# Performance work log

Measured on AMD Instinct MI355X. Metric: run time of the kernel, lower is better.

The kernel has to match this reference:

```python
import jax, jax.numpy as jnp
import numpy as np

B, N, DEG = 16, 2048, 16          # graphs, nodes per graph, avg out-degree
C_IN, HID, K = 64, 128, 32        # in_channels, hidden_channels, out_channels (clusters)
NT = B * N                        # total nodes
E = NT * DEG                      # total edges
GN_EPS = 1e-5


def setup_inputs() -> dict:
    key = jax.random.key(0)
    ks = jax.random.split(key, 6)
    x = jax.random.normal(ks[0], (NT, C_IN), jnp.float32)
    # within-graph random edges (sorted batch => node i belongs to graph i // N)
    src_l = jax.random.randint(ks[1], (E,), 0, N)
    dst_l = jax.random.randint(ks[2], (E,), 0, N)
    gid = jnp.repeat(jnp.arange(B, dtype=jnp.int32), N * DEG)
    edge_index = jnp.stack([gid * N + src_l, gid * N + dst_l]).astype(jnp.int32)
    batch = jnp.repeat(jnp.arange(B, dtype=jnp.int32), N)
    return dict(
        x=x, edge_index=edge_index, batch=batch,
        gn_weight=jnp.ones((C_IN,), jnp.float32),
        gn_bias=jnp.zeros((C_IN,), jnp.float32),
        gn_mean_scale=jnp.ones((C_IN,), jnp.float32),
        w1=jax.random.normal(ks[3], (C_IN, HID), jnp.float32) / np.float32(np.sqrt(C_IN)),
        b1=jnp.zeros((HID,), jnp.float32),
        w2=jax.random.normal(ks[4], (HID, K), jnp.float32) / np.float32(np.sqrt(HID)),
        b2=jnp.zeros((K,), jnp.float32),
    )


def reference(x, gn_weight, gn_bias, gn_mean_scale, w1, b1, w2, b2, edge_index, batch):
    # ---- GraphNorm (per-graph mean/var with learnable mean scale) ----
    ones_n = jnp.ones((NT,), x.dtype)
    cnt = jax.ops.segment_sum(ones_n, batch, num_segments=B)[:, None]        # [B,1]
    mean = jax.ops.segment_sum(x, batch, num_segments=B) / cnt              # [B,C]
    xm = x - gn_mean_scale * mean[batch]
    var = jax.ops.segment_sum(xm * xm, batch, num_segments=B) / cnt         # [B,C]
    h = gn_weight * xm / jnp.sqrt(var + GN_EPS)[batch] + gn_bias            # [NT,C_IN]

    # ---- GCNConv (add self-loops, symmetric D^-1/2 (A+I) D^-1/2) ----
    src, dst = edge_index[0], edge_index[1]
    loop = jnp.arange(NT, dtype=src.dtype)
    src_l = jnp.concatenate([src, loop])
    dst_l = jnp.concatenate([dst, loop])
    deg = jax.ops.segment_sum(jnp.ones_like(src_l, x.dtype), dst_l, num_segments=NT)
    dinv = jnp.where(deg > 0, jax.lax.rsqrt(deg), 0.0)
    norm = dinv[src_l] * dinv[dst_l]                                        # [E+NT]
    hw = h @ w1                                                             # [NT,HID]
    h = jax.ops.segment_sum(norm[:, None] * hw[src_l], dst_l, num_segments=NT) + b1
    h = jax.nn.selu(h)

    # ---- to_dense_batch / to_dense_adj (uniform graph sizes -> mask all True) ----
    xd = h.reshape(B, N, HID)                                               # [B,N,F]
    adj = jnp.zeros((B, N, N), x.dtype).at[batch[src], src % N, dst % N].add(1.0)

    # ---- DMoNPooling ----
    s = jax.nn.softmax(xd @ w2 + b2, axis=-1)                               # [B,N,K]
    out = jax.nn.selu(jnp.einsum('bnk,bnf->bkf', s, xd))                    # [B,K,F]
    sta = jnp.einsum('bnk,bnm->bkm', s, adj)                                # [B,K,N]
    out_adj = jnp.einsum('bkm,bml->bkl', sta, s)                            # [B,K,K]

    degrees = adj.sum(-1)                                                   # [B,N]
    m = degrees.sum(-1) / 2                                                 # [B]
    ca = jnp.einsum('bnk,bn->bk', s, degrees)                               # [B,K]
    normalizer = ca[:, :, None] * ca[:, None, :] / 2 / m[:, None, None]
    spectral_loss = (-jnp.einsum('bkk->b', out_adj - normalizer) / (2 * m)).mean()

    ss = jnp.einsum('bnk,bnl->bkl', s, s)                                   # [B,K,K]
    ss_fro = jnp.sqrt(jnp.sum(ss * ss, axis=(-2, -1), keepdims=True))
    eye = jnp.eye(K, dtype=x.dtype)
    diff = ss / ss_fro - eye / jnp.sqrt(jnp.float32(K))
    ortho_loss = jnp.sqrt(jnp.sum(diff * diff, axis=(-2, -1))).mean()

    cluster_size = s.sum(1)                                                 # [B,K]
    cluster_loss = (jnp.linalg.norm(cluster_size, axis=1) / N
                    * jnp.sqrt(jnp.float32(K)) - 1).mean()
    # (coarsened-adj renormalization in DMoNPooling is unused by Net's outputs)

    return jax.nn.log_softmax(out, axis=-1), spectral_loss + ortho_loss + cluster_loss, s
```

## Files before the change

kernel.cpp:

```cpp
#include <hip/hip_runtime.h>
#include <cmath>

static constexpr int B_  = 16;
static constexpr int N_  = 2048;
static constexpr int NT_ = 32768;
static constexpr int E_  = 524288;

static constexpr size_t OFF_HSC    = 0;
static constexpr size_t OFF_XD     = 2097152;
static constexpr size_t OFF_SWS    = 6291456;
static constexpr size_t OFF_PART   = 7340032;
static constexpr size_t OFF_GSP    = 9437184;
static constexpr size_t OFF_GSP2   = 9445376;
static constexpr size_t OFF_SSP    = 9453568;
static constexpr size_t OFF_CAP    = 9977856;
static constexpr size_t OFF_CSP    = 9994240;
static constexpr size_t OFF_SPECP  = 10010624;
static constexpr size_t OFF_DINV   = 10011136;
static constexpr size_t OFF_IHIN   = 10043904;
static constexpr size_t OFF_IHOUT  = 10306048;
static constexpr size_t OFF_ICURS  = 10568192;
static constexpr size_t OFF_IROWS  = 10830336;
static constexpr size_t OFF_ICNTO  = 10863108;
static constexpr size_t OFF_IESRC  = 10895876;

__device__ __forceinline__ float selu_f(float x) {
  return 1.0507009873554805f * (x > 0.f ? x : 1.6732632423543772f * expm1f(x));
}

__device__ __forceinline__ float block_sum_bcast(float v, float* sm) {
  int lane = threadIdx.x & 63, w = threadIdx.x >> 6;
#pragma unroll
  for (int off = 32; off; off >>= 1) v += __shfl_down(v, off);
  __syncthreads();
  if (lane == 0) sm[w] = v;
  __syncthreads();
  return sm[0] + sm[1] + sm[2] + sm[3];
}

__global__ __launch_bounds__(1024) void k_count(const int* ei, const float* x,
                                                int* histin, int* histout,
                                                float* gsp, float* gsp2) {
  __shared__ int hin[2048], hout[2048];
  __shared__ float l1[16][64], l2[16][64];
  int blk = blockIdx.x;
  int tid = threadIdx.x;
  if (blk < 128) {
    int g = blk >> 3, p = blk & 7;
    int nbase = g * 2048, ebase = g * 32768 + p * 4096;
    hin[tid] = 0; hin[tid + 1024] = 0;
    hout[tid] = 0; hout[tid + 1024] = 0;
    __syncthreads();
#pragma unroll
    for (int it = 0; it < 4; it++) {
      int e = ebase + it * 1024 + tid;
      int s = ei[e], d = ei[E_ + e];
      atomicAdd(&hout[s - nbase], 1);
      atomicAdd(&hin[d - nbase], 1);
    }
    __syncthreads();
    histin[blk * 2048 + tid] = hin[tid];
    histin[blk * 2048 + tid + 1024] = hin[tid + 1024];
    histout[blk * 2048 + tid] = hout[tid];
    histout[blk * 2048 + tid + 1024] = hout[tid + 1024];
  } else {
    int gi = blk - 128;
    int b = gi >> 3, chunk = gi & 7;
    int c = tid & 63, r = tid >> 6;
    float s = 0.f, s2 = 0.f;
    const float* xb = x + ((size_t)b * N_ + (size_t)chunk * 256) * 64;
    for (int n = r; n < 256; n += 16) {
      float v = xb[n * 64 + c];
      s += v; s2 += v * v;
    }
    l1[r][c] = s; l2[r][c] = s2;
    __syncthreads();
    if (r == 0) {
      float t1 = 0.f, t2 = 0.f;
#pragma unroll
      for (int i = 0; i < 16; i++) { t1 += l1[i][c]; t2 += l2[i][c]; }
      gsp[gi * 64 + c] = t1;
      gsp2[gi * 64 + c] = t2;
    }
  }
}

__global__ __launch_bounds__(1024) void k_scan(const int* histin, const int* histout,
                                               int* rows, int* cursp, int* cout_,
                                               float* dinv) {
  __shared__ int sb[1024];
  int g = blockIdx.x, tid = threadIdx.x;
  int nbase = g * 2048, ebase = g * 32768;
  int n0 = 2 * tid, n1 = 2 * tid + 1;
  int h0[8], h1[8];
  int a = 0, b = 0, o0 = 0, o1 = 0;
#pragma unroll
  for (int p = 0; p < 8; p++) {
    h0[p] = histin[(g * 8 + p) * 2048 + n0];
    h1[p] = histin[(g * 8 + p) * 2048 + n1];
    a += h0[p]; b += h1[p];
    o0 += histout[(g * 8 + p) * 2048 + n0];
    o1 += histout[(g * 8 + p) * 2048 + n1];
  }
  sb[tid] = a + b;
  __syncthreads();
  for (int off = 1; off < 1024; off <<= 1) {
    int add = (tid >= off) ? sb[tid - off] : 0;
    __syncthreads();
    sb[tid] += add;
    __syncthreads();
  }
  int pref = (tid > 0) ? sb[tid - 1] : 0;
  int r0 = ebase + pref, r1 = r0 + a;
  rows[nbase + n0] = r0;
  rows[nbase + n1] = r1;
  dinv[nbase + n0] = rsqrtf((float)(a + 1));
  dinv[nbase + n1] = rsqrtf((float)(b + 1));
  cout_[nbase + n0] = o0;
  cout_[nbase + n1] = o1;
  int run0 = r0, run1 = r1;
#pragma unroll
  for (int p = 0; p < 8; p++) {
    cursp[(g * 8 + p) * 2048 + n0] = run0; run0 += h0[p];
    cursp[(g * 8 + p) * 2048 + n1] = run1; run1 += h1[p];
  }
  if (g == 15 && tid == 1023) rows[NT_] = E_;
}

__global__ __launch_bounds__(256) void k_prepb(const float* x, const float* gsp,
                                               const float* gsp2, const float* gw,
                                               const float* gb, const float* gms,
                                               const float* dinv, float* hsc,
                                               const int* ei, const int* cursp,
                                               int* esrc) {
  __shared__ float shs[64], scs[64];
  __shared__ int cur[2048];
  int tid = threadIdx.x;
  int blk = blockIdx.x;
  if (blk < 2048) {
    int bgr = blk >> 7;
    if (tid < 64) {
      float s = 0.f, s2 = 0.f;
#pragma unroll
      for (int c8 = 0; c8 < 8; c8++) {
        s  += gsp[(bgr * 8 + c8) * 64 + tid];
        s2 += gsp2[(bgr * 8 + c8) * 64 + tid];
      }
      float mean = s * (1.f / 2048.f);
      float a = gms[tid];
      float var = s2 * (1.f / 2048.f) - (2.f * a - a * a) * mean * mean;
      shs[tid] = a * mean;
      scs[tid] = gw[tid] * rsqrtf(var + 1e-5f);
    }
    __syncthreads();
    int idx = blk * 256 + tid;
    int node = idx >> 4, g4 = (idx & 15) * 4;
    float di = dinv[node];
    float4 xv = *(const float4*)&x[(size_t)node * 64 + g4];
    float4 bb = *(const float4*)&gb[g4];
    float4 o;
    o.x = ((xv.x - shs[g4])     * scs[g4]     + bb.x) * di;
    o.y = ((xv.y - shs[g4 + 1]) * scs[g4 + 1] + bb.y) * di;
    o.z = ((xv.z - shs[g4 + 2]) * scs[g4 + 2] + bb.z) * di;
    o.w = ((xv.w - shs[g4 + 3]) * scs[g4 + 3] + bb.w) * di;
    *(float4*)&hsc[(size_t)node * 64 + g4] = o;
  } else {
    int bb = blk - 2048;
    int g = bb >> 3, p = bb & 7;
    int nbase = g * 2048;
    int ebase = g * 32768 + p * 4096;
    for (int i = tid; i < 2048; i += 256) cur[i] = cursp[bb * 2048 + i];
    __syncthreads();
#pragma unroll
    for (int it = 0; it < 16; it++) {
      int e = ebase + it * 256 + tid;
      int s = ei[e], d = ei[E_ + e];
      int pos = atomicAdd(&cur[d - nbase], 1);
      esrc[pos] = s;
    }
  }
}

__global__ __launch_bounds__(256) void k_mm1(const float* hsc, const float* dinv,
                                             const int* rows, const int* esrc,
                                             const float* w1, const float* b1,
                                             float* xd) {
  __shared__ float at[32 * 65];
  int tid = threadIdx.x;
  int n0 = blockIdx.x * 32;
  int wv = tid >> 6, c = tid & 63;
#pragma unroll 1
  for (int i = 0; i < 8; i++) {
    int nn = i * 4 + wv;
    int node = n0 + nn;
    int e0 = rows[node], e1 = rows[node + 1];
    float dd = dinv[node];
    float acc = hsc[(size_t)node * 64 + c];
    for (int e = e0; e < e1; e += 8) {
      int sidx[8]; float wt[8], hv[8];
#pragma unroll
      for (int j = 0; j < 8; j++) {
        int ee = e + j;
        sidx[j] = esrc[ee < e1 ? ee : e0];
        wt[j] = (ee < e1) ? 1.f : 0.f;
      }
#pragma unroll
      for (int j = 0; j < 8; j++) hv[j] = hsc[(size_t)sidx[j] * 64 + c];
#pragma unroll
      for (int j = 0; j < 8; j++) acc += wt[j] * hv[j];
    }
    at[nn * 65 + c] = dd * acc;
  }
  __syncthreads();
  int tx = tid & 31, ty = tid >> 5;
  int f0 = tx * 4, nn = ty * 4;
  float acc[4][4] = {};
  for (int k = 0; k < 64; k++) {
    float4 wvv = *(const float4*)&w1[k * 128 + f0];
#pragma unroll
    for (int i = 0; i < 4; i++) {
      float av = at[(nn + i) * 65 + k];
      acc[i][0] += av * wvv.x; acc[i][1] += av * wvv.y;
      acc[i][2] += av * wvv.z; acc[i][3] += av * wvv.w;
    }
  }
  float4 bv = *(const float4*)&b1[f0];
#pragma unroll
  for (int i = 0; i < 4; i++) {
    float4 o;
    o.x = selu_f(acc[i][0] + bv.x);
    o.y = selu_f(acc[i][1] + bv.y);
    o.z = selu_f(acc[i][2] + bv.z);
    o.w = selu_f(acc[i][3] + bv.w);
    *(float4*)&xd[(size_t)(n0 + nn + i) * 128 + f0] = o;
  }
}

__global__ __launch_bounds__(256) void k_mm2f(const float* xd, const float* w2,
                                              const float* b2, const int* cout_,
                                              float* s_ws, float* outs, float* ssp,
                                              float* cap, float* csp, float* part) {
  __shared__ float xt[64 * 129];
  __shared__ float st[64 * 33];
  __shared__ float r1[8][32], r2[8][32];
  int tid = threadIdx.x;
  int blk = blockIdx.x;
  int n0 = blk * 64;
  for (int i = tid; i < 2048; i += 256) {
    int n = i >> 5, j4 = (i & 31) * 4;
    float4 v = *(const float4*)&xd[(size_t)(n0 + n) * 128 + j4];
    xt[n * 129 + j4] = v.x; xt[n * 129 + j4 + 1] = v.y;
    xt[n * 129 + j4 + 2] = v.z; xt[n * 129 + j4 + 3] = v.w;
  }
  __syncthreads();
  int ty = tid >> 3;
  int k0 = (tid & 7) * 4;
  float acc2[2][4] = {};
  for (int j = 0; j < 128; j++) {
    float4 wv = *(const float4*)&w2[j * 32 + k0];
    float x0 = xt[(ty * 2) * 129 + j];
    float x1 = xt[(ty * 2 + 1) * 129 + j];
    acc2[0][0] += x0 * wv.x; acc2[0][1] += x0 * wv.y; acc2[0][2] += x0 * wv.z; acc2[0][3] += x0 * wv.w;
    acc2[1][0] += x1 * wv.x; acc2[1][1] += x1 * wv.y; acc2[1][2] += x1 * wv.z; acc2[1][3] += x1 * wv.w;
  }
  float4 bv2 = *(const float4*)&b2[k0];
#pragma unroll
  for (int i = 0; i < 2; i++) {
    int n = ty * 2 + i;
    st[n * 33 + k0]     = acc2[i][0] + bv2.x;
    st[n * 33 + k0 + 1] = acc2[i][1] + bv2.y;
    st[n * 33 + k0 + 2] = acc2[i][2] + bv2.z;
    st[n * 33 + k0 + 3] = acc2[i][3] + bv2.w;
  }
  __syncthreads();
  if (tid < 64) {
    float m = -3.4e38f;
    for (int kk = 0; kk < 32; kk++) m = fmaxf(m, st[tid * 33 + kk]);
    float ssum = 0.f;
    for (int kk = 0; kk < 32; kk++) {
      float e = expf(st[tid * 33 + kk] - m);
      st[tid * 33 + kk] = e; ssum += e;
    }
    float inv = 1.f / ssum;
    for (int kk = 0; kk < 32; kk++) st[tid * 33 + kk] *= inv;
  }
  __syncthreads();
  for (int i = tid; i < 512; i += 256) {
    int n = i >> 3, q = (i & 7) * 4;
    float4 o = {st[n * 33 + q], st[n * 33 + q + 1], st[n * 33 + q + 2], st[n * 33 + q + 3]};
    *(float4*)&s_ws[(size_t)(n0 + n) * 32 + q] = o;
    float* op = &outs[(size_t)(n0 + n) * 32 + q];
    op[0] = o.x; op[1] = o.y; op[2] = o.z; op[3] = o.w;
  }
  {
    int k = tid >> 3, l0 = (tid & 7) * 4;
    float a0 = 0, a1 = 0, a2 = 0, a3 = 0;
    for (int n = 0; n < 64; n++) {
      float sk = st[n * 33 + k];
      a0 += sk * st[n * 33 + l0];     a1 += sk * st[n * 33 + l0 + 1];
      a2 += sk * st[n * 33 + l0 + 2]; a3 += sk * st[n * 33 + l0 + 3];
    }
    float4 o = {a0, a1, a2, a3};
    *(float4*)&ssp[(size_t)blk * 1024 + k * 32 + l0] = o;
  }
  {
    int k2 = tid & 31, r = tid >> 5;
    float aca = 0.f, acs = 0.f;
    for (int i = 0; i < 8; i++) {
      int n = i * 8 + r;
      float dg = (float)cout_[n0 + n];
      float v = st[n * 33 + k2];
      acs += v; aca += v * dg;
    }
    r1[r][k2] = aca; r2[r][k2] = acs;
    __syncthreads();
    if (r == 0) {
      float sa = 0.f, sc = 0.f;
#pragma unroll
      for (int i = 0; i < 8; i++) { sa += r1[i][k2]; sc += r2[i][k2]; }
      cap[blk * 32 + k2] = sa;
      csp[blk * 32 + k2] = sc;
    }
  }
  {
    int tx = tid & 31, ty2 = tid >> 5;
    int f0 = tx * 4, kk0 = ty2 * 4;
    float acc[4][4] = {};
    for (int n = 0; n < 64; n++) {
      float s0 = st[n * 33 + kk0], s1 = st[n * 33 + kk0 + 1];
      float s2 = st[n * 33 + kk0 + 2], s3 = st[n * 33 + kk0 + 3];
      float4 xv = {xt[n * 129 + f0], xt[n * 129 + f0 + 1], xt[n * 129 + f0 + 2], xt[n * 129 + f0 + 3]};
      acc[0][0] += s0 * xv.x; acc[0][1] += s0 * xv.y; acc[0][2] += s0 * xv.z; acc[0][3] += s0 * xv.w;
      acc[1][0] += s1 * xv.x; acc[1][1] += s1 * xv.y; acc[1][2] += s1 * xv.z; acc[1][3] += s1 * xv.w;
      acc[2][0] += s2 * xv.x; acc[2][1] += s2 * xv.y; acc[2][2] += s2 * xv.z; acc[2][3] += s2 * xv.w;
      acc[3][0] += s3 * xv.x; acc[3][1] += s3 * xv.y; acc[3][2] += s3 * xv.z; acc[3][3] += s3 * xv.w;
    }
#pragma unroll
    for (int i = 0; i < 4; i++) {
      float4 o = {acc[i][0], acc[i][1], acc[i][2], acc[i][3]};
      *(float4*)&part[(size_t)(blk * 32 + kk0 + i) * 128 + f0] = o;
    }
  }
}

__global__ __launch_bounds__(256) void k_spec(const int* ei, const float* s_ws,
                                              float* specp, float* lossp) {
  __shared__ float sm4[4];
  int blk = blockIdx.x, tid = threadIdx.x;
  if (blk == 0 && tid == 0) lossp[0] = 0.f;
  int ebase = blk * 1024;
  float acc = 0.f;
#pragma unroll
  for (int j = 0; j < 4; j++) {
    int e = ebase + j * 256 + tid;
    int s = ei[e], d = ei[E_ + e];
    const float4* ap = (const float4*)&s_ws[(size_t)s * 32];
    const float4* cp = (const float4*)&s_ws[(size_t)d * 32];
#pragma unroll
    for (int q = 0; q < 8; q++) {
      float4 u = ap[q], v = cp[q];
      acc += u.x * v.x + u.y * v.y + u.z * v.z + u.w * v.w;
    }
  }
  int lane = tid & 63, w = tid >> 6;
#pragma unroll
  for (int off = 32; off; off >>= 1) acc += __shfl_down(acc, off);
  if (lane == 0) sm4[w] = acc;
  __syncthreads();
  if (tid == 0) specp[blk] = sm4[0] + sm4[1] + sm4[2] + sm4[3];
}

__global__ __launch_bounds__(256) void k_fin2(const float* part, const float* ssp,
                                              const float* csp, const float* cap,
                                              const float* specp, float* out0,
                                              float* loss) {
  __shared__ float sred[4];
  int blk = blockIdx.x;
  int tid = threadIdx.x;
  if (blk < 256) {
    int half = tid >> 7;
    int f = tid & 127;
    int row = blk * 2 + half;
    int b = row >> 5, k = row & 31;
    float v = 0.f;
#pragma unroll
    for (int c = 0; c < 32; c++) v += part[(size_t)((b * 32 + c) * 32 + k) * 128 + f];
    v = selu_f(v);
    int lane = tid & 63, w = tid >> 6;
    float m = v;
#pragma unroll
    for (int off = 32; off; off >>= 1) m = fmaxf(m, __shfl_down(m, off));
    if (lane == 0) sred[w] = m;
    __syncthreads();
    m = fmaxf(sred[half * 2], sred[half * 2 + 1]);
    float e = expf(v - m);
    float t = e;
    __syncthreads();
#pragma unroll
    for (int off = 32; off; off >>= 1) t += __shfl_down(t, off);
    if (lane == 0) sred[w] = t;
    __syncthreads();
    float tot = sred[half * 2] + sred[half * 2 + 1];
    out0[(size_t)row * 128 + f] = v - m - logf(tot);
  } else {
    int b = blk - 256;
    float v0 = 0, v1 = 0, v2 = 0, v3 = 0;
    for (int c = 0; c < 32; c++) {
      float4 u = *(const float4*)&ssp[(size_t)(b * 32 + c) * 1024 + tid * 4];
      v0 += u.x; v1 += u.y; v2 += u.z; v3 += u.w;
    }
    float ssq = v0 * v0 + v1 * v1 + v2 * v2 + v3 * v3;
    ssq = block_sum_bcast(ssq, sred);
    float inv = 1.f / sqrtf(ssq);
    float dsq = 0.f;
    {
      int i0 = tid * 4;
      float vv[4] = {v0, v1, v2, v3};
#pragma unroll
      for (int jj = 0; jj < 4; jj++) {
        int i = i0 + jj;
        float d = vv[jj] * inv;
        if ((i >> 5) == (i & 31)) d -= 0.17677669529663687f;
        dsq += d * d;
      }
    }
    dsq = block_sum_bcast(dsq, sred);
    float csq = 0.f, casq = 0.f;
    if (tid < 32) {
      float c1 = 0.f, c2 = 0.f;
      for (int c = 0; c < 32; c++) {
        c1 += csp[(size_t)(b * 32 + c) * 32 + tid];
        c2 += cap[(size_t)(b * 32 + c) * 32 + tid];
      }
      csq = c1 * c1; casq = c2 * c2;
    }
    csq = block_sum_bcast(csq, sred);
    casq = block_sum_bcast(casq, sred);
    float spec_sum = (tid < 32) ? specp[b * 32 + tid] : 0.f;
    spec_sum = block_sum_bcast(spec_sum, sred);
    if (tid == 0) {
      float ortho = sqrtf(dsq);
      float cl = sqrtf(csq) * (1.f / 2048.f) * 5.656854249492381f - 1.f;
      float m = 16384.f;
      float spec = -(spec_sum - casq / (2.f * m)) / (2.f * m);
      atomicAdd(loss, (spec + ortho + cl) * (1.f / 16.f));
    }
  }
}

extern "C" void kernel_launch(void* const* d_in, const int* in_sizes, int n_in,
                              void* d_out, int out_size, void* d_ws, size_t ws_size,
                              hipStream_t stream) {
  (void)in_sizes; (void)n_in; (void)out_size; (void)ws_size;
  const float* x   = (const float*)d_in[0];
  const int*   ei  = (const int*)d_in[1];
  const float* gw  = (const float*)d_in[3];
  const float* gb  = (const float*)d_in[4];
  const float* gms = (const float*)d_in[5];
  const float* w1  = (const float*)d_in[6];
  const float* b1  = (const float*)d_in[7];
  const float* w2  = (const float*)d_in[8];
  const float* b2  = (const float*)d_in[9];
  float* out = (float*)d_out;
  float* ws  = (float*)d_ws;

  float* hsc    = ws + OFF_HSC;
  float* xd     = ws + OFF_XD;
  float* s_ws   = ws + OFF_SWS;
  float* part   = ws + OFF_PART;
  float* gsp    = ws + OFF_GSP;
  float* gsp2   = ws + OFF_GSP2;
  float* ssp    = ws + OFF_SSP;
  float* cap    = ws + OFF_CAP;
  float* csp    = ws + OFF_CSP;
  float* specp  = ws + OFF_SPECP;
  float* dinv   = ws + OFF_DINV;
  int*   histin = (int*)(ws + OFF_IHIN);
  int*   histout= (int*)(ws + OFF_IHOUT);
  int*   cursp  = (int*)(ws + OFF_ICURS);
  int*   rows   = (int*)(ws + OFF_IROWS);
  int*   cout_  = (int*)(ws + OFF_ICNTO);
  int*   esrc   = (int*)(ws + OFF_IESRC);

  float* out0  = out;
  float* lossp = out + 65536;
  float* outs  = out + 65537;

  hipLaunchKernelGGL(k_count, dim3(256), dim3(1024), 0, stream, ei, x, histin, histout, gsp, gsp2);
  hipLaunchKernelGGL(k_scan, dim3(16), dim3(1024), 0, stream,
                     histin, histout, rows, cursp, cout_, dinv);
  hipLaunchKernelGGL(k_prepb, dim3(2176), dim3(256), 0, stream,
                     x, gsp, gsp2, gw, gb, gms, dinv, hsc, ei, cursp, esrc);
  hipLaunchKernelGGL(k_mm1, dim3(1024), dim3(256), 0, stream, hsc, dinv, rows, esrc, w1, b1, xd);
  hipLaunchKernelGGL(k_mm2f, dim3(512), dim3(256), 0, stream,
                     xd, w2, b2, cout_, s_ws, outs, ssp, cap, csp, part);
  hipLaunchKernelGGL(k_spec, dim3(512), dim3(256), 0, stream, ei, s_ws, specp, lossp);
  hipLaunchKernelGGL(k_fin2, dim3(272), dim3(256), 0, stream,
                     part, ssp, csp, cap, specp, out0, lossp);
}
```

Measured before the change: 203.5 us.

## Fuse GCN aggregation+W1 matmul with W2/softmax/pooling kernel via shared memory

```diff
diff --git a/kernel.cpp b/kernel.cpp
--- a/kernel.cpp
+++ b/kernel.cpp
@@ -7,22 +7,21 @@
 static constexpr int E_  = 524288;
 
 static constexpr size_t OFF_HSC    = 0;
-static constexpr size_t OFF_XD     = 2097152;
-static constexpr size_t OFF_SWS    = 6291456;
-static constexpr size_t OFF_PART   = 7340032;
-static constexpr size_t OFF_GSP    = 9437184;
-static constexpr size_t OFF_GSP2   = 9445376;
-static constexpr size_t OFF_SSP    = 9453568;
-static constexpr size_t OFF_CAP    = 9977856;
-static constexpr size_t OFF_CSP    = 9994240;
-static constexpr size_t OFF_SPECP  = 10010624;
-static constexpr size_t OFF_DINV   = 10011136;
-static constexpr size_t OFF_IHIN   = 10043904;
-static constexpr size_t OFF_IHOUT  = 10306048;
-static constexpr size_t OFF_ICURS  = 10568192;
-static constexpr size_t OFF_IROWS  = 10830336;
-static constexpr size_t OFF_ICNTO  = 10863108;
-static constexpr size_t OFF_IESRC  = 10895876;
+static constexpr size_t OFF_SWS    = 2097152;
+static constexpr size_t OFF_PART   = 3145728;
+static constexpr size_t OFF_GSP    = 5242880;
+static constexpr size_t OFF_GSP2   = 5251072;
+static constexpr size_t OFF_SSP    = 5259264;
+static constexpr size_t OFF_CAP    = 5783552;
+static constexpr size_t OFF_CSP    = 5799936;
+static constexpr size_t OFF_SPECP  = 5816320;
+static constexpr size_t OFF_DINV   = 5816832;
+static constexpr size_t OFF_IHIN   = 5849600;
+static constexpr size_t OFF_IHOUT  = 6111744;
+static constexpr size_t OFF_ICURS  = 6373888;
+static constexpr size_t OFF_IROWS  = 6636032;
+static constexpr size_t OFF_ICNTO  = 6668804;
+static constexpr size_t OFF_IESRC  = 6701572;
 
 __device__ __forceinline__ float selu_f(float x) {
   return 1.0507009873554805f * (x > 0.f ? x : 1.6732632423543772f * expm1f(x));
@@ -181,17 +180,24 @@
   }
 }
 
-__global__ __launch_bounds__(256) void k_mm1(const float* hsc, const float* dinv,
-                                             const int* rows, const int* esrc,
-                                             const float* w1, const float* b1,
-                                             float* xd) {
-  __shared__ float at[32 * 65];
+__global__ __launch_bounds__(512) void k_mm12(const float* hsc, const float* dinv,
+                                              const int* rows, const int* esrc,
+                                              const float* w1, const float* b1,
+                                              const float* w2, const float* b2,
+                                              const int* cout_, float* s_ws,
+                                              float* outs, float* ssp, float* cap,
+                                              float* csp, float* part) {
+  __shared__ float xt[64 * 129];
+  __shared__ float at[64 * 65];
+  __shared__ float st[64 * 33];
+  __shared__ float r1[16][32], r2[16][32];
   int tid = threadIdx.x;
-  int n0 = blockIdx.x * 32;
+  int blk = blockIdx.x;
+  int n0 = blk * 64;
   int wv = tid >> 6, c = tid & 63;
 #pragma unroll 1
   for (int i = 0; i < 8; i++) {
-    int nn = i * 4 + wv;
+    int nn = i * 8 + wv;
     int node = n0 + nn;
     int e0 = rows[node], e1 = rows[node + 1];
     float dd = dinv[node];
@@ -212,65 +218,43 @@
     at[nn * 65 + c] = dd * acc;
   }
   __syncthreads();
-  int tx = tid & 31, ty = tid >> 5;
-  int f0 = tx * 4, nn = ty * 4;
-  float acc[4][4] = {};
-  for (int k = 0; k < 64; k++) {
-    float4 wvv = *(const float4*)&w1[k * 128 + f0];
+  {
+    int tx = tid & 31, ty = tid >> 5;
+    int f0 = tx * 4, nn = ty * 4;
+    float acc[4][4] = {};
+    for (int k = 0; k < 64; k++) {
+      float4 wvv = *(const float4*)&w1[k * 128 + f0];
+#pragma unroll
+      for (int i = 0; i < 4; i++) {
+        float av = at[(nn + i) * 65 + k];
+        acc[i][0] += av * wvv.x; acc[i][1] += av * wvv.y;
+        acc[i][2] += av * wvv.z; acc[i][3] += av * wvv.w;
+      }
+    }
+    float4 bv = *(const float4*)&b1[f0];
 #pragma unroll
     for (int i = 0; i < 4; i++) {
-      float av = at[(nn + i) * 65 + k];
-      acc[i][0] += av * wvv.x; acc[i][1] += av * wvv.y;
-      acc[i][2] += av * wvv.z; acc[i][3] += av * wvv.w;
-    }
-  }
-  float4 bv = *(const float4*)&b1[f0];
-#pragma unroll
-  for (int i = 0; i < 4; i++) {
-    float4 o;
-    o.x = selu_f(acc[i][0] + bv.x);
-    o.y = selu_f(acc[i][1] + bv.y);
-    o.z = selu_f(acc[i][2] + bv.z);
-    o.w = selu_f(acc[i][3] + bv.w);
-    *(float4*)&xd[(size_t)(n0 + nn + i) * 128 + f0] = o;
-  }
-}
-
-__global__ __launch_bounds__(256) void k_mm2f(const float* xd, const float* w2,
-                                              const float* b2, const int* cout_,
-                                              float* s_ws, float* outs, float* ssp,
-                                              float* cap, float* csp, float* part) {
-  __shared__ float xt[64 * 129];
-  __shared__ float st[64 * 33];
-  __shared__ float r1[8][32], r2[8][32];
-  int tid = threadIdx.x;
-  int blk = blockIdx.x;
-  int n0 = blk * 64;
-  for (int i = tid; i < 2048; i += 256) {
-    int n = i >> 5, j4 = (i & 31) * 4;
-    float4 v = *(const float4*)&xd[(size_t)(n0 + n) * 128 + j4];
-    xt[n * 129 + j4] = v.x; xt[n * 129 + j4 + 1] = v.y;
-    xt[n * 129 + j4 + 2] = v.z; xt[n * 129 + j4 + 3] = v.w;
-  }
-  __syncthreads();
-  int ty = tid >> 3;
-  int k0 = (tid & 7) * 4;
-  float acc2[2][4] = {};
-  for (int j = 0; j < 128; j++) {
-    float4 wv = *(const float4*)&w2[j * 32 + k0];
-    float x0 = xt[(ty * 2) * 129 + j];
-    float x1 = xt[(ty * 2 + 1) * 129 + j];
-    acc2[0][0] += x0 * wv.x; acc2[0][1] += x0 * wv.y; acc2[0][2] += x0 * wv.z; acc2[0][3] += x0 * wv.w;
-    acc2[1][0] += x1 * wv.x; acc2[1][1] += x1 * wv.y; acc2[1][2] += x1 * wv.z; acc2[1][3] += x1 * wv.w;
-  }
-  float4 bv2 = *(const float4*)&b2[k0];
-#pragma unroll
-  for (int i = 0; i < 2; i++) {
-    int n = ty * 2 + i;
-    st[n * 33 + k0]     = acc2[i][0] + bv2.x;
-    st[n * 33 + k0 + 1] = acc2[i][1] + bv2.y;
-    st[n * 33 + k0 + 2] = acc2[i][2] + bv2.z;
-    st[n * 33 + k0 + 3] = acc2[i][3] + bv2.w;
+      xt[(nn + i) * 129 + f0]     = selu_f(acc[i][0] + bv.x);
+      xt[(nn + i) * 129 + f0 + 1] = selu_f(acc[i][1] + bv.y);
+      xt[(nn + i) * 129 + f0 + 2] = selu_f(acc[i][2] + bv.z);
+      xt[(nn + i) * 129 + f0 + 3] = selu_f(acc[i][3] + bv.w);
+    }
+  }
+  __syncthreads();
+  {
+    int ty = tid >> 3;
+    int k0 = (tid & 7) * 4;
+    float a4[4] = {};
+    for (int j = 0; j < 128; j++) {
+      float4 wvv = *(const float4*)&w2[j * 32 + k0];
+      float xv = xt[ty * 129 + j];
+      a4[0] += xv * wvv.x; a4[1] += xv * wvv.y; a4[2] += xv * wvv.z; a4[3] += xv * wvv.w;
+    }
+    float4 bv2 = *(const float4*)&b2[k0];
+    st[ty * 33 + k0]     = a4[0] + bv2.x;
+    st[ty * 33 + k0 + 1] = a4[1] + bv2.y;
+    st[ty * 33 + k0 + 2] = a4[2] + bv2.z;
+    st[ty * 33 + k0 + 3] = a4[3] + bv2.w;
   }
   __syncthreads();
   if (tid < 64) {
@@ -285,29 +269,30 @@
     for (int kk = 0; kk < 32; kk++) st[tid * 33 + kk] *= inv;
   }
   __syncthreads();
-  for (int i = tid; i < 512; i += 256) {
-    int n = i >> 3, q = (i & 7) * 4;
+  {
+    int n = tid >> 3, q = (tid & 7) * 4;
     float4 o = {st[n * 33 + q], st[n * 33 + q + 1], st[n * 33 + q + 2], st[n * 33 + q + 3]};
     *(float4*)&s_ws[(size_t)(n0 + n) * 32 + q] = o;
     float* op = &outs[(size_t)(n0 + n) * 32 + q];
     op[0] = o.x; op[1] = o.y; op[2] = o.z; op[3] = o.w;
   }
   {
-    int k = tid >> 3, l0 = (tid & 7) * 4;
-    float a0 = 0, a1 = 0, a2 = 0, a3 = 0;
+    int k = tid >> 4, l0 = (tid & 15) * 2;
+    float a0 = 0.f, a1 = 0.f;
     for (int n = 0; n < 64; n++) {
       float sk = st[n * 33 + k];
-      a0 += sk * st[n * 33 + l0];     a1 += sk * st[n * 33 + l0 + 1];
-      a2 += sk * st[n * 33 + l0 + 2]; a3 += sk * st[n * 33 + l0 + 3];
-    }
-    float4 o = {a0, a1, a2, a3};
-    *(float4*)&ssp[(size_t)blk * 1024 + k * 32 + l0] = o;
+      a0 += sk * st[n * 33 + l0];
+      a1 += sk * st[n * 33 + l0 + 1];
+    }
+    ssp[(size_t)blk * 1024 + k * 32 + l0]     = a0;
+    ssp[(size_t)blk * 1024 + k * 32 + l0 + 1] = a1;
   }
   {
     int k2 = tid & 31, r = tid >> 5;
     float aca = 0.f, acs = 0.f;
-    for (int i = 0; i < 8; i++) {
-      int n = i * 8 + r;
+#pragma unroll
+    for (int i = 0; i < 4; i++) {
+      int n = i * 16 + r;
       float dg = (float)cout_[n0 + n];
       float v = st[n * 33 + k2];
       acs += v; aca += v * dg;
@@ -317,26 +302,24 @@
     if (r == 0) {
       float sa = 0.f, sc = 0.f;
 #pragma unroll
-      for (int i = 0; i < 8; i++) { sa += r1[i][k2]; sc += r2[i][k2]; }
+      for (int i = 0; i < 16; i++) { sa += r1[i][k2]; sc += r2[i][k2]; }
       cap[blk * 32 + k2] = sa;
       csp[blk * 32 + k2] = sc;
     }
   }
   {
     int tx = tid & 31, ty2 = tid >> 5;
-    int f0 = tx * 4, kk0 = ty2 * 4;
-    float acc[4][4] = {};
+    int f0 = tx * 4, kk0 = ty2 * 2;
+    float acc[2][4] = {};
     for (int n = 0; n < 64; n++) {
       float s0 = st[n * 33 + kk0], s1 = st[n * 33 + kk0 + 1];
-      float s2 = st[n * 33 + kk0 + 2], s3 = st[n * 33 + kk0 + 3];
-      float4 xv = {xt[n * 129 + f0], xt[n * 129 + f0 + 1], xt[n * 129 + f0 + 2], xt[n * 129 + f0 + 3]};
-      acc[0][0] += s0 * xv.x; acc[0][1] += s0 * xv.y; acc[0][2] += s0 * xv.z; acc[0][3] += s0 * xv.w;
-      acc[1][0] += s1 * xv.x; acc[1][1] += s1 * xv.y; acc[1][2] += s1 * xv.z; acc[1][3] += s1 * xv.w;
-      acc[2][0] += s2 * xv.x; acc[2][1] += s2 * xv.y; acc[2][2] += s2 * xv.z; acc[2][3] += s2 * xv.w;
-      acc[3][0] += s3 * xv.x; acc[3][1] += s3 * xv.y; acc[3][2] += s3 * xv.z; acc[3][3] += s3 * xv.w;
-    }
-#pragma unroll
-    for (int i = 0; i < 4; i++) {
+      float x0 = xt[n * 129 + f0],     x1 = xt[n * 129 + f0 + 1];
+      float x2 = xt[n * 129 + f0 + 2], x3 = xt[n * 129 + f0 + 3];
+      acc[0][0] += s0 * x0; acc[0][1] += s0 * x1; acc[0][2] += s0 * x2; acc[0][3] += s0 * x3;
+      acc[1][0] += s1 * x0; acc[1][1] += s1 * x1; acc[1][2] += s1 * x2; acc[1][3] += s1 * x3;
+    }
+#pragma unroll
+    for (int i = 0; i < 2; i++) {
       float4 o = {acc[i][0], acc[i][1], acc[i][2], acc[i][3]};
       *(float4*)&part[(size_t)(blk * 32 + kk0 + i) * 128 + f0] = o;
     }
@@ -465,7 +448,6 @@
   float* ws  = (float*)d_ws;
 
   float* hsc    = ws + OFF_HSC;
-  float* xd     = ws + OFF_XD;
   float* s_ws   = ws + OFF_SWS;
   float* part   = ws + OFF_PART;
   float* gsp    = ws + OFF_GSP;
@@ -491,9 +473,9 @@
                      histin, histout, rows, cursp, cout_, dinv);
   hipLaunchKernelGGL(k_prepb, dim3(2176), dim3(256), 0, stream,
                      x, gsp, gsp2, gw, gb, gms, dinv, hsc, ei, cursp, esrc);
-  hipLaunchKernelGGL(k_mm1, dim3(1024), dim3(256), 0, stream, hsc, dinv, rows, esrc, w1, b1, xd);
-  hipLaunchKernelGGL(k_mm2f, dim3(512), dim3(256), 0, stream,
-                     xd, w2, b2, cout_, s_ws, outs, ssp, cap, csp, part);
+  hipLaunchKernelGGL(k_mm12, dim3(512), dim3(512), 0, stream,
+                     hsc, dinv, rows, esrc, w1, b1, w2, b2, cout_,
+                     s_ws, outs, ssp, cap, csp, part);
   hipLaunchKernelGGL(k_spec, dim3(512), dim3(256), 0, stream, ei, s_ws, specp, lossp);
   hipLaunchKernelGGL(k_fin2, dim3(272), dim3(256), 0, stream,
                      part, ssp, csp, cap, specp, out0, lossp);
```

Measured after the change: 208.1 us. 1.02x slower.
